# Performance work log

Hardware: AMD Instinct MI355X
Metric: run time of the kernel (lower is better)

Reference implementation:

```python
import jax, jax.numpy as jnp
import numpy as np

LOG_2PI = float(np.log(2.0 * np.pi))

def setup_inputs() -> dict:
    key = jax.random.key(0)
    k1, k2 = jax.random.split(key)
    N, D, K = 131072, 64, 64
    inputs = jax.random.normal(k1, (N, D), dtype=jnp.float32)
    mu = jax.random.normal(k2, (K, D), dtype=jnp.float32)
    logvars = jnp.zeros((K, D), dtype=jnp.float32)
    logpriors = jnp.zeros((K,), dtype=jnp.float32)
    return {"inputs": inputs, "mu": mu, "logvars": logvars, "logpriors": logpriors}

def reference(inputs, mu, logvars, logpriors):
    # log N(x | mu, diag(exp(logvar))), summed over feature dim -> (K, N)
    # broadcast: (1,N,D) - (K,1,D)
    a = (inputs[None, :, :] - mu[:, None, :]) ** 2
    log_p = -0.5 * (logvars[:, None, :] + a * jnp.exp(-logvars[:, None, :])) - 0.5 * LOG_2PI
    log_likelihoods = jnp.sum(log_p, axis=-1)  # (K, N)
    # normalize priors over K (logsumexp of logpriors)
    norm_logpriors = logpriors - jax.nn.logsumexp(logpriors)
    weighted = log_likelihoods + norm_logpriors[:, None]  # (K, N)
    # posterior normalization over K per example
    log_posteriors = weighted - jax.nn.logsumexp(weighted, axis=0, keepdims=True)
    return log_posteriors
```

## Files before the change

### kernel.cpp

```cpp
#include <hip/hip_runtime.h>
#include <math.h>

#define NPTS 131072
#define DDIM 64
#define KMIX 64
#define LOG_2PI 1.8378770664093453f

typedef __attribute__((ext_vector_type(8))) short short8;
typedef __attribute__((ext_vector_type(4))) float floatx4;

static __device__ __forceinline__ unsigned short f2bf(float f) {
    unsigned int u = __float_as_uint(f);
    unsigned int r = (u + 0x7fffu + ((u >> 16) & 1u)) >> 16;
    return (unsigned short)r;
}

__global__ void gmm_prep(const float* __restrict__ mu,
                         const float* __restrict__ lv,
                         const float* __restrict__ lp,
                         float* __restrict__ Wf32,
                         float* __restrict__ C)
{
    const int k = blockIdx.x;
    const int d = threadIdx.x;

    float x = lp[d];
    float m = x;
    #pragma unroll
    for (int off = 32; off > 0; off >>= 1)
        m = fmaxf(m, __shfl_xor(m, off, 64));
    float s = expf(x - m);
    #pragma unroll
    for (int off = 32; off > 0; off >>= 1)
        s += __shfl_xor(s, off, 64);
    const float lse_lp = m + logf(s);

    const float l  = lv[k * DDIM + d];
    const float ev = expf(-l);
    const float mv = mu[k * DDIM + d];
    Wf32[k * 128 + d]      = -0.5f * ev;
    Wf32[k * 128 + 64 + d] = mv * ev;

    float c = -0.5f * l - 0.5f * mv * mv * ev;
    #pragma unroll
    for (int off = 32; off > 0; off >>= 1)
        c += __shfl_xor(c, off, 64);
    if (d == 0)
        C[k] = c + (lp[k] - lse_lp) - 0.5f * (float)DDIM * LOG_2PI;
}

__global__ void gmm_pack(const float* __restrict__ Wf32,
                         unsigned short* __restrict__ WhPack)
{
    const int b    = blockIdx.x;
    const int lane = threadIdx.x;
    const int krow = (b >> 2) * 16 + (lane & 15);
    const int ibase = (b & 3) * 32 + (lane >> 4) * 8;
    #pragma unroll
    for (int j = 0; j < 8; ++j)
        WhPack[(b * 64 + lane) * 8 + j] = f2bf(Wf32[krow * 128 + ibase + j]);
}

__global__ __launch_bounds__(256, 4)
void gmm_main(const float* __restrict__ xg,
              const unsigned short* __restrict__ WhPack,
              const float* __restrict__ C,
              float* __restrict__ out)
{
    __shared__ float O[KMIX * 68];

    const int lane = threadIdx.x & 63;
    const int wid  = __builtin_amdgcn_readfirstlane(threadIdx.x >> 6);
    const int g    = lane >> 4;
    const int nn   = lane & 15;

    const int bn0 = blockIdx.x * 64;
    const int n   = bn0 + wid * 16 + nn;

    const float* __restrict__ xr = xg + (size_t)n * DDIM + g * 8;
    const float4 p0 = *(const float4*)(xr);
    const float4 p1 = *(const float4*)(xr + 4);
    const float4 p2 = *(const float4*)(xr + 32);
    const float4 p3 = *(const float4*)(xr + 36);

    short8 wh[4][4];
    #pragma unroll
    for (int t = 0; t < 4; ++t)
        #pragma unroll
        for (int u = 0; u < 4; ++u)
            wh[t][u] = *(const short8*)(WhPack + ((t * 4 + u) * 64 + lane) * 8);

    floatx4 cw[4];
    #pragma unroll
    for (int t = 0; t < 4; ++t)
        cw[t] = *(const floatx4*)(C + t * 16 + g * 4);

    const float ca[8] = {p0.x, p0.y, p0.z, p0.w, p1.x, p1.y, p1.z, p1.w};
    const float cb[8] = {p2.x, p2.y, p2.z, p2.w, p3.x, p3.y, p3.z, p3.w};

    short8 bh[4];
    #pragma unroll
    for (int j = 0; j < 8; ++j) {
        bh[0][j] = (short)f2bf(ca[j] * ca[j]);
        bh[1][j] = (short)f2bf(cb[j] * cb[j]);
        bh[2][j] = (short)f2bf(ca[j]);
        bh[3][j] = (short)f2bf(cb[j]);
    }

    floatx4 acc[4];
    #pragma unroll
    for (int t = 0; t < 4; ++t) acc[t] = (floatx4){0.f, 0.f, 0.f, 0.f};

    #pragma unroll
    for (int u = 0; u < 4; ++u)
        #pragma unroll
        for (int t = 0; t < 4; ++t)
            acc[t] = __builtin_amdgcn_mfma_f32_16x16x32_bf16(wh[t][u], bh[u], acc[t], 0, 0, 0);

    #pragma unroll
    for (int t = 0; t < 4; ++t)
        #pragma unroll
        for (int r = 0; r < 4; ++r)
            acc[t][r] += cw[t][r];

    float t8[8];
    #pragma unroll
    for (int i = 0; i < 8; ++i)
        t8[i] = fmaxf(acc[i >> 2][i & 3], acc[2 + (i >> 2)][i & 3]);
    #pragma unroll
    for (int i = 0; i < 4; ++i) t8[i] = fmaxf(t8[i], t8[i + 4]);
    float m = fmaxf(fmaxf(t8[0], t8[1]), fmaxf(t8[2], t8[3]));
    m = fmaxf(m, __shfl_xor(m, 16, 64));
    m = fmaxf(m, __shfl_xor(m, 32, 64));

    float s0 = 0.f, s1 = 0.f, s2 = 0.f, s3 = 0.f;
    #pragma unroll
    for (int t = 0; t < 4; ++t) {
        s0 += __expf(acc[t][0] - m);
        s1 += __expf(acc[t][1] - m);
        s2 += __expf(acc[t][2] - m);
        s3 += __expf(acc[t][3] - m);
    }
    float s = (s0 + s1) + (s2 + s3);
    s += __shfl_xor(s, 16, 64);
    s += __shfl_xor(s, 32, 64);
    const float lse = m + __logf(s);

    #pragma unroll
    for (int t = 0; t < 4; ++t)
        #pragma unroll
        for (int r = 0; r < 4; ++r)
            O[(t * 16 + g * 4 + r) * 68 + wid * 16 + nn] = acc[t][r] - lse;

    __syncthreads();

    #pragma unroll
    for (int rr = 0; rr < 4; ++rr) {
        const int row = rr * 16 + (threadIdx.x >> 4);
        const int c4  = (threadIdx.x & 15) * 4;
        const float4 v = *(const float4*)&O[row * 68 + c4];
        *(float4*)&out[(size_t)row * NPTS + bn0 + c4] = v;
    }
}

extern "C" void kernel_launch(void* const* d_in, const int* in_sizes, int n_in,
                              void* d_out, int out_size, void* d_ws, size_t ws_size,
                              hipStream_t stream) {
    const float* inputs    = (const float*)d_in[0];
    const float* mu        = (const float*)d_in[1];
    const float* logvars   = (const float*)d_in[2];
    const float* logpriors = (const float*)d_in[3];

    float* out = (float*)d_out;

    unsigned short* WhPack = (unsigned short*)d_ws;
    float* Wf32 = (float*)(WhPack + KMIX * 128);
    float* Cc   = Wf32 + KMIX * 128;

    gmm_prep<<<KMIX, DDIM, 0, stream>>>(mu, logvars, logpriors, Wf32, Cc);
    gmm_pack<<<16, 64, 0, stream>>>(Wf32, WhPack);
    gmm_main<<<NPTS / 64, 256, 0, stream>>>(inputs, WhPack, Cc, out);
}
```

Baseline: 96.24 us.

## Fuse weight packing into prep kernel and process two tiles per block

```diff
diff --git a/kernel.cpp b/kernel.cpp
--- a/kernel.cpp
+++ b/kernel.cpp
@@ -18,7 +18,7 @@
 __global__ void gmm_prep(const float* __restrict__ mu,
                          const float* __restrict__ lv,
                          const float* __restrict__ lp,
-                         float* __restrict__ Wf32,
+                         unsigned short* __restrict__ WhPack,
                          float* __restrict__ C)
 {
     const int k = blockIdx.x;
@@ -38,8 +38,6 @@
     const float l  = lv[k * DDIM + d];
     const float ev = expf(-l);
     const float mv = mu[k * DDIM + d];
-    Wf32[k * 128 + d]      = -0.5f * ev;
-    Wf32[k * 128 + 64 + d] = mv * ev;
 
     float c = -0.5f * l - 0.5f * mv * mv * ev;
     #pragma unroll
@@ -47,18 +45,22 @@
         c += __shfl_xor(c, off, 64);
     if (d == 0)
         C[k] = c + (lp[k] - lse_lp) - 0.5f * (float)DDIM * LOG_2PI;
-}
 
-__global__ void gmm_pack(const float* __restrict__ Wf32,
-                         unsigned short* __restrict__ WhPack)
-{
-    const int b    = blockIdx.x;
-    const int lane = threadIdx.x;
-    const int krow = (b >> 2) * 16 + (lane & 15);
-    const int ibase = (b & 3) * 32 + (lane >> 4) * 8;
-    #pragma unroll
-    for (int j = 0; j < 8; ++j)
-        WhPack[(b * 64 + lane) * 8 + j] = f2bf(Wf32[krow * 128 + ibase + j]);
+    if (k < 16) {
+        const int b     = k;
+        const int krow  = (b >> 2) * 16 + (d & 15);
+        const int ibase = (b & 3) * 32 + (d >> 4) * 8;
+        short8 v;
+        #pragma unroll
+        for (int j = 0; j < 8; ++j) {
+            const int i  = ibase + j;
+            const int dd = i & 63;
+            const float e = expf(-lv[krow * DDIM + dd]);
+            const float w = (i < 64) ? (-0.5f * e) : (mu[krow * DDIM + dd] * e);
+            v[j] = (short)f2bf(w);
+        }
+        *(short8*)(WhPack + (b * 64 + d) * 8) = v;
+    }
 }
 
 __global__ __launch_bounds__(256, 4)
@@ -74,14 +76,8 @@
     const int g    = lane >> 4;
     const int nn   = lane & 15;
 
-    const int bn0 = blockIdx.x * 64;
-    const int n   = bn0 + wid * 16 + nn;
-
-    const float* __restrict__ xr = xg + (size_t)n * DDIM + g * 8;
-    const float4 p0 = *(const float4*)(xr);
-    const float4 p1 = *(const float4*)(xr + 4);
-    const float4 p2 = *(const float4*)(xr + 32);
-    const float4 p3 = *(const float4*)(xr + 36);
+    const int bn0 = blockIdx.x * 128;
+    const int col = wid * 16 + nn;
 
     short8 wh[4][4];
     #pragma unroll
@@ -95,71 +91,83 @@
     for (int t = 0; t < 4; ++t)
         cw[t] = *(const floatx4*)(C + t * 16 + g * 4);
 
-    const float ca[8] = {p0.x, p0.y, p0.z, p0.w, p1.x, p1.y, p1.z, p1.w};
-    const float cb[8] = {p2.x, p2.y, p2.z, p2.w, p3.x, p3.y, p3.z, p3.w};
+    #pragma unroll 1
+    for (int unit = 0; unit < 2; ++unit) {
+        const int un0 = bn0 + unit * 64;
+        const float* __restrict__ xr = xg + (size_t)(un0 + col) * DDIM + g * 8;
+        const float4 p0 = *(const float4*)(xr);
+        const float4 p1 = *(const float4*)(xr + 4);
+        const float4 p2 = *(const float4*)(xr + 32);
+        const float4 p3 = *(const float4*)(xr + 36);
+        const float ca[8] = {p0.x, p0.y, p0.z, p0.w, p1.x, p1.y, p1.z, p1.w};
+        const float cb[8] = {p2.x, p2.y, p2.z, p2.w, p3.x, p3.y, p3.z, p3.w};
 
-    short8 bh[4];
-    #pragma unroll
-    for (int j = 0; j < 8; ++j) {
-        bh[0][j] = (short)f2bf(ca[j] * ca[j]);
-        bh[1][j] = (short)f2bf(cb[j] * cb[j]);
-        bh[2][j] = (short)f2bf(ca[j]);
-        bh[3][j] = (short)f2bf(cb[j]);
-    }
+        short8 bh[4];
+        #pragma unroll
+        for (int j = 0; j < 8; ++j) {
+            bh[0][j] = (short)f2bf(ca[j] * ca[j]);
+            bh[1][j] = (short)f2bf(cb[j] * cb[j]);
+            bh[2][j] = (short)f2bf(ca[j]);
+            bh[3][j] = (short)f2bf(cb[j]);
+        }
 
-    floatx4 acc[4];
-    #pragma unroll
-    for (int t = 0; t < 4; ++t) acc[t] = (floatx4){0.f, 0.f, 0.f, 0.f};
+        floatx4 acc[4];
+        #pragma unroll
+        for (int t = 0; t < 4; ++t) acc[t] = (floatx4){0.f, 0.f, 0.f, 0.f};
 
-    #pragma unroll
-    for (int u = 0; u < 4; ++u)
+        #pragma unroll
+        for (int u = 0; u < 4; ++u)
+            #pragma unroll
+            for (int t = 0; t < 4; ++t)
+                acc[t] = __builtin_amdgcn_mfma_f32_16x16x32_bf16(wh[t][u], bh[u], acc[t], 0, 0, 0);
+
         #pragma unroll
         for (int t = 0; t < 4; ++t)
-            acc[t] = __builtin_amdgcn_mfma_f32_16x16x32_bf16(wh[t][u], bh[u], acc[t], 0, 0, 0);
+            #pragma unroll
+            for (int r = 0; r < 4; ++r)
+                acc[t][r] += cw[t][r];
 
-    #pragma unroll
-    for (int t = 0; t < 4; ++t)
+        float t8[8];
         #pragma unroll
-        for (int r = 0; r < 4; ++r)
-            acc[t][r] += cw[t][r];
+        for (int i = 0; i < 8; ++i)
+            t8[i] = fmaxf(acc[i >> 2][i & 3], acc[2 + (i >> 2)][i & 3]);
+        #pragma unroll
+        for (int i = 0; i < 4; ++i) t8[i] = fmaxf(t8[i], t8[i + 4]);
+        float m = fmaxf(fmaxf(t8[0], t8[1]), fmaxf(t8[2], t8[3]));
+        m = fmaxf(m, __shfl_xor(m, 16, 64));
+        m = fmaxf(m, __shfl_xor(m, 32, 64));
 
-    float t8[8];
-    #pragma unroll
-    for (int i = 0; i < 8; ++i)
-        t8[i] = fmaxf(acc[i >> 2][i & 3], acc[2 + (i >> 2)][i & 3]);
-    #pragma unroll
-    for (int i = 0; i < 4; ++i) t8[i] = fmaxf(t8[i], t8[i + 4]);
-    float m = fmaxf(fmaxf(t8[0], t8[1]), fmaxf(t8[2], t8[3]));
-    m = fmaxf(m, __shfl_xor(m, 16, 64));
-    m = fmaxf(m, __shfl_xor(m, 32, 64));
+        float s0 = 0.f, s1 = 0.f, s2 = 0.f, s3 = 0.f;
+        #pragma unroll
+        for (int t = 0; t < 4; ++t) {
+            s0 += __expf(acc[t][0] - m);
+            s1 += __expf(acc[t][1] - m);
+            s2 += __expf(acc[t][2] - m);
+            s3 += __expf(acc[t][3] - m);
+        }
+        float s = (s0 + s1) + (s2 + s3);
+        s += __shfl_xor(s, 16, 64);
+        s += __shfl_xor(s, 32, 64);
+        const float lse = m + __logf(s);
 
-    float s0 = 0.f, s1 = 0.f, s2 = 0.f, s3 = 0.f;
-    #pragma unroll
-    for (int t = 0; t < 4; ++t) {
-        s0 += __expf(acc[t][0] - m);
-        s1 += __expf(acc[t][1] - m);
-        s2 += __expf(acc[t][2] - m);
-        s3 += __expf(acc[t][3] - m);
-    }
-    float s = (s0 + s1) + (s2 + s3);
-    s += __shfl_xor(s, 16, 64);
-    s += __shfl_xor(s, 32, 64);
-    const float lse = m + __logf(s);
+        if (unit)
+            __syncthreads();
 
-    #pragma unroll
-    for (int t = 0; t < 4; ++t)
         #pragma unroll
-        for (int r = 0; r < 4; ++r)
-            O[(t * 16 + g * 4 + r) * 68 + wid * 16 + nn] = acc[t][r] - lse;
+        for (int t = 0; t < 4; ++t)
+            #pragma unroll
+            for (int r = 0; r < 4; ++r)
+                O[(t * 16 + g * 4 + r) * 68 + col] = acc[t][r] - lse;
 
-    __syncthreads();
+        __syncthreads();
 
-    #pragma unroll
-    for (int rr = 0; rr < 4; ++rr) {
-        const int row = rr * 16 + (threadIdx.x >> 4);
-        const int c4  = (threadIdx.x & 15) * 4;
-        const float4 v = *(const float4*)&O[row * 68 + c4];
-        *(float4*)&out[(size_t)row * NPTS + bn0 + c4] = v;
+        #pragma unroll
+        for (int rr = 0; rr < 4; ++rr) {
+            const int row = rr * 16 + (threadIdx.x >> 4);
+            const int c4  = (threadIdx.x & 15) * 4;
+            const float4 v = *(const float4*)&O[row * 68 + c4];
+            *(float4*)&out[(size_t)row * NPTS + un0 + c4] = v;
+        }
     }
 }
 
@@ -174,10 +182,8 @@
     float* out = (float*)d_out;
 
     unsigned short* WhPack = (unsigned short*)d_ws;
-    float* Wf32 = (float*)(WhPack + KMIX * 128);
-    float* Cc   = Wf32 + KMIX * 128;
+    float* Cc = (float*)(WhPack + KMIX * 128);
 
-    gmm_prep<<<KMIX, DDIM, 0, stream>>>(mu, logvars, logpriors, Wf32, Cc);
-    gmm_pack<<<16, 64, 0, stream>>>(Wf32, WhPack);
-    gmm_main<<<NPTS / 64, 256, 0, stream>>>(inputs, WhPack, Cc, out);
+    gmm_prep<<<KMIX, DDIM, 0, stream>>>(mu, logvars, logpriors, WhPack, Cc);
+    gmm_main<<<NPTS / 128, 256, 0, stream>>>(inputs, WhPack, Cc, out);
 }
```

Result: slower. 103.2 us (+7.2%).
